# Kernel tuning notes

Hardware: AMD Instinct MI355X
Metric: run time of the kernel (lower is better)

The kernel has to match this reference:

```python
import jax, jax.numpy as jnp
import numpy as np
from jax import lax

IN_CH, OUT_CH, K = 64, 64, 3
FAN_IN = 8           # LogicNets-style fan-in per output channel (over C_in*K taps)
IN_SCALE, IN_BITS = 0.0625, 8
OUT_SCALE, OUT_BITS = 0.125, 8


def make_mask(seed=7):
    # Binary mask [OUT_CH, IN_CH, K] with exactly FAN_IN ones per output channel
    rng = np.random.RandomState(seed)
    m = np.zeros((OUT_CH, IN_CH * K), dtype=np.float32)
    for o in range(OUT_CH):
        idx = rng.choice(IN_CH * K, size=FAN_IN, replace=False)
        m[o, idx] = 1.0
    return jnp.asarray(m.reshape(OUT_CH, IN_CH, K))


def fake_quant(v, scale, bits):
    # symmetric fake quantization with straight-through estimator
    qmin = -(2 ** (bits - 1))
    qmax = 2 ** (bits - 1) - 1
    q = jnp.clip(jnp.round(v / scale), qmin, qmax) * scale
    return v + lax.stop_gradient(q - v)


def setup_inputs() -> dict:
    key = jax.random.key(0)
    k1, k2 = jax.random.split(key)
    x = jax.random.normal(k1, (512, IN_CH, 1024), dtype=jnp.float32)
    weight = jax.random.normal(k2, (OUT_CH, IN_CH, K), dtype=jnp.float32) * 0.1
    mask = make_mask()
    return {"x": x, "weight": weight, "mask": mask}


def reference(x, weight, mask):
    # input quant
    xq = fake_quant(x, IN_SCALE, IN_BITS)
    # masked (sparse) conv1d, padding=1 (same length)
    w = weight * mask
    out = lax.conv_general_dilated(
        xq, w,
        window_strides=(1,),
        padding=[(1, 1)],
        dimension_numbers=("NCH", "OIH", "NCH"),
    )
    # output quant
    return fake_quant(out, OUT_SCALE, OUT_BITS)
```

## Files before the change

kernel.cpp:

```cpp
#include <hip/hip_runtime.h>

namespace {
constexpr int kInCh  = 64;
constexpr int kOutCh = 64;
constexpr int kK     = 3;
constexpr int kFanIn = 8;
constexpr int kH     = 1024;
constexpr int kTile  = 64;
constexpr int kRow   = 72;
constexpr int kWaves = 4;
constexpr int kBlk   = 64 * kWaves;
constexpr int kHB    = kH / kTile;
constexpr int kGridB = 512;
}

struct Tap { int off; float w; };

__device__ __forceinline__ float quant_in_i(float v) {
    float q = rintf(v * 16.0f);
    q = fmaxf(q, -128.0f);
    return fminf(q, 127.0f);
}

__device__ __forceinline__ float quant_out(float v) {
    float q = rintf(v * 8.0f);
    q = fmaxf(q, -128.0f);
    q = fminf(q, 127.0f);
    return q * 0.125f;
}

__global__ void prep_taps(const float* __restrict__ weight,
                          const float* __restrict__ mask,
                          Tap* __restrict__ taps) {
    __shared__ unsigned long long bal[3];
    const int o    = blockIdx.x;
    const int j    = threadIdx.x;
    const int k    = j >> 6;
    const int ci   = j & 63;
    const int idx  = (o * kInCh + ci) * kK + k;

    const float m = mask[idx];
    const unsigned long long b = __ballot(m != 0.0f);
    if (ci == 0) bal[k] = b;
    __syncthreads();

    const unsigned long long lower = b & ((1ull << ci) - 1ull);
    int rank = __popcll(lower);
    #pragma unroll
    for (int w = 0; w < kK; ++w) if (w < k) rank += __popcll(bal[w]);

    if (m != 0.0f && rank < kFanIn) {
        taps[o * kFanIn + rank].off = ci * kRow + k + 3;
        taps[o * kFanIn + rank].w   = weight[idx] * m * 0.0625f;
    }
    int total = __popcll(bal[0]) + __popcll(bal[1]) + __popcll(bal[2]);
    if (j >= total && j < kFanIn) {
        taps[o * kFanIn + j].off = 3;
        taps[o * kFanIn + j].w   = 0.0f;
    }
}

__device__ __forceinline__ void issue_loads(const float* __restrict__ x, int tau,
                                            int lane, float4* __restrict__ r,
                                            float& hl, float& hr) {
    const int n  = tau >> 4;
    const int h0 = (tau & (kHB - 1)) * kTile;
    const float* __restrict__ p = x + ((size_t)n * kInCh) * kH + h0;
    #pragma unroll
    for (int i = 0; i < 16; ++i) {
        const int f = i * 64 + lane;
        r[i] = reinterpret_cast<const float4*>(p + (f >> 4) * kH)[f & 15];
    }
    hl = 0.f; hr = 0.f;
    if (h0 > 0)          hl = p[lane * kH - 1];
    if (h0 + kTile < kH) hr = p[lane * kH + kTile];
}

__device__ __forceinline__ void stage(float (* __restrict__ my)[kRow], int lane,
                                      const float4* __restrict__ r, float hl, float hr) {
    #pragma unroll
    for (int i = 0; i < 16; ++i) {
        const int f = i * 64 + lane;
        float4 q;
        q.x = quant_in_i(r[i].x); q.y = quant_in_i(r[i].y);
        q.z = quant_in_i(r[i].z); q.w = quant_in_i(r[i].w);
        *reinterpret_cast<float4*>(&my[f >> 4][4 + (f & 15) * 4]) = q;
    }
    my[lane][3]         = quant_in_i(hl);
    my[lane][4 + kTile] = quant_in_i(hr);
}

__global__ __launch_bounds__(kBlk, 2) void sparse_conv(
        const float* __restrict__ x,
        const Tap*   __restrict__ taps,
        float*       __restrict__ out,
        int nTiles, int strideW) {
    __shared__ float sm[kWaves][kInCh][kRow];

    const int t    = threadIdx.x;
    const int lane = t & 63;
    const int g    = __builtin_amdgcn_readfirstlane(t >> 6);
    float (* __restrict__ my)[kRow] = sm[g];
    const float* __restrict__ smf = &my[0][0];

    int tau = blockIdx.x * kWaves + g;
    float4 r[16]; float hl, hr;
    if (tau < nTiles) issue_loads(x, tau, lane, r, hl, hr);

    while (tau < nTiles) {
        stage(my, lane, r, hl, hr);
        const int cur = tau;
        tau += strideW;
        if (tau < nTiles) issue_loads(x, tau, lane, r, hl, hr);

        const int n  = cur >> 4;
        const int h0 = (cur & (kHB - 1)) * kTile;
        float* __restrict__ outn = out + ((size_t)n * kOutCh) * kH + h0;

        #pragma unroll 8
        for (int o = 0; o < kOutCh; ++o) {
            const Tap* __restrict__ tp = taps + o * kFanIn;
            float acc = 0.f;
            #pragma unroll
            for (int j = 0; j < kFanIn; ++j)
                acc = fmaf(tp[j].w, smf[tp[j].off + lane], acc);
            outn[(size_t)o * kH + lane] = quant_out(acc);
        }
    }
}

extern "C" void kernel_launch(void* const* d_in, const int* in_sizes, int n_in,
                              void* d_out, int out_size, void* d_ws, size_t ws_size,
                              hipStream_t stream) {
    const float* x      = (const float*)d_in[0];
    const float* weight = (const float*)d_in[1];
    const float* mask   = (const float*)d_in[2];
    float* out = (float*)d_out;
    Tap* taps = (Tap*)d_ws;

    const int nBatch = in_sizes[0] / (kInCh * kH);
    const int nTiles = nBatch * kHB;
    const int strideW = kGridB * kWaves;

    prep_taps<<<kOutCh, kInCh * kK, 0, stream>>>(weight, mask, taps);
    sparse_conv<<<kGridB, kBlk, 0, stream>>>(x, taps, out, nTiles, strideW);
}
```

Measured before the change: 255.6 us.

## Share each input tile across a 512-thread block, splitting output channels over waves

```diff
diff --git a/kernel.cpp b/kernel.cpp
--- a/kernel.cpp
+++ b/kernel.cpp
@@ -8,10 +8,9 @@
 constexpr int kH     = 1024;
 constexpr int kTile  = 64;
 constexpr int kRow   = 72;
-constexpr int kWaves = 4;
-constexpr int kBlk   = 64 * kWaves;
+constexpr int kBlk   = 512;
 constexpr int kHB    = kH / kTile;
-constexpr int kGridB = 512;
+constexpr int kGridB = 2048;
 }
 
 struct Tap { int off; float w; };
@@ -60,73 +59,73 @@
     }
 }
 
-__device__ __forceinline__ void issue_loads(const float* __restrict__ x, int tau,
-                                            int lane, float4* __restrict__ r,
-                                            float& hl, float& hr) {
-    const int n  = tau >> 4;
-    const int h0 = (tau & (kHB - 1)) * kTile;
-    const float* __restrict__ p = x + ((size_t)n * kInCh) * kH + h0;
-    #pragma unroll
-    for (int i = 0; i < 16; ++i) {
-        const int f = i * 64 + lane;
-        r[i] = reinterpret_cast<const float4*>(p + (f >> 4) * kH)[f & 15];
-    }
-    hl = 0.f; hr = 0.f;
-    if (h0 > 0)          hl = p[lane * kH - 1];
-    if (h0 + kTile < kH) hr = p[lane * kH + kTile];
-}
-
-__device__ __forceinline__ void stage(float (* __restrict__ my)[kRow], int lane,
-                                      const float4* __restrict__ r, float hl, float hr) {
-    #pragma unroll
-    for (int i = 0; i < 16; ++i) {
-        const int f = i * 64 + lane;
-        float4 q;
-        q.x = quant_in_i(r[i].x); q.y = quant_in_i(r[i].y);
-        q.z = quant_in_i(r[i].z); q.w = quant_in_i(r[i].w);
-        *reinterpret_cast<float4*>(&my[f >> 4][4 + (f & 15) * 4]) = q;
-    }
-    my[lane][3]         = quant_in_i(hl);
-    my[lane][4 + kTile] = quant_in_i(hr);
-}
-
-__global__ __launch_bounds__(kBlk, 2) void sparse_conv(
+__global__ __launch_bounds__(kBlk, 8) void sparse_conv(
         const float* __restrict__ x,
         const Tap*   __restrict__ taps,
         float*       __restrict__ out,
-        int nTiles, int strideW) {
-    __shared__ float sm[kWaves][kInCh][kRow];
+        int nTiles, int stride) {
+    __shared__ float sm[2][kInCh * kRow];
 
     const int t    = threadIdx.x;
     const int lane = t & 63;
     const int g    = __builtin_amdgcn_readfirstlane(t >> 6);
-    float (* __restrict__ my)[kRow] = sm[g];
-    const float* __restrict__ smf = &my[0][0];
+    const int ci0  = t >> 4;
+    const int c4   = t & 15;
 
-    int tau = blockIdx.x * kWaves + g;
-    float4 r[16]; float hl, hr;
-    if (tau < nTiles) issue_loads(x, tau, lane, r, hl, hr);
+    float4 r0, r1; float hl = 0.f;
+    int tau = blockIdx.x;
+
+#define ISSUE(TAU)                                                                 \
+    {                                                                              \
+        const int n_  = (TAU) >> 4;                                                \
+        const int h0_ = ((TAU) & (kHB - 1)) * kTile;                               \
+        const float* __restrict__ p_ = x + ((size_t)n_ * kInCh) * kH + h0_;        \
+        r0 = reinterpret_cast<const float4*>(p_ + ci0 * kH)[c4];                   \
+        r1 = reinterpret_cast<const float4*>(p_ + (ci0 + 32) * kH)[c4];            \
+        hl = 0.f;                                                                  \
+        if (t < 64)       { if (h0_ > 0)          hl = p_[t * kH - 1]; }           \
+        else if (t < 128) { if (h0_ + kTile < kH) hl = p_[(t - 64) * kH + kTile]; }\
+    }
+
+    ISSUE(tau);
+    int p = 0;
 
     while (tau < nTiles) {
-        stage(my, lane, r, hl, hr);
+        float* __restrict__ buf = sm[p];
+        {
+            float4 q;
+            q.x = quant_in_i(r0.x); q.y = quant_in_i(r0.y);
+            q.z = quant_in_i(r0.z); q.w = quant_in_i(r0.w);
+            reinterpret_cast<float4*>(&buf[ci0 * kRow + 4])[c4] = q;
+            q.x = quant_in_i(r1.x); q.y = quant_in_i(r1.y);
+            q.z = quant_in_i(r1.z); q.w = quant_in_i(r1.w);
+            reinterpret_cast<float4*>(&buf[(ci0 + 32) * kRow + 4])[c4] = q;
+            if (t < 64)       buf[t * kRow + 3] = quant_in_i(hl);
+            else if (t < 128) buf[(t - 64) * kRow + 4 + kTile] = quant_in_i(hl);
+        }
+        __syncthreads();
+
         const int cur = tau;
-        tau += strideW;
-        if (tau < nTiles) issue_loads(x, tau, lane, r, hl, hr);
+        tau += stride;
+        if (tau < nTiles) ISSUE(tau);
 
         const int n  = cur >> 4;
         const int h0 = (cur & (kHB - 1)) * kTile;
         float* __restrict__ outn = out + ((size_t)n * kOutCh) * kH + h0;
 
-        #pragma unroll 8
-        for (int o = 0; o < kOutCh; ++o) {
+        #pragma unroll 4
+        for (int oo = 0; oo < 8; ++oo) {
+            const int o = g * 8 + oo;
             const Tap* __restrict__ tp = taps + o * kFanIn;
             float acc = 0.f;
             #pragma unroll
             for (int j = 0; j < kFanIn; ++j)
-                acc = fmaf(tp[j].w, smf[tp[j].off + lane], acc);
+                acc = fmaf(tp[j].w, buf[tp[j].off + lane], acc);
             outn[(size_t)o * kH + lane] = quant_out(acc);
         }
+        p ^= 1;
     }
+#undef ISSUE
 }
 
 extern "C" void kernel_launch(void* const* d_in, const int* in_sizes, int n_in,
@@ -140,8 +139,8 @@
 
     const int nBatch = in_sizes[0] / (kInCh * kH);
     const int nTiles = nBatch * kHB;
-    const int strideW = kGridB * kWaves;
+    const int grid   = nTiles < kGridB ? nTiles : kGridB;
 
     prep_taps<<<kOutCh, kInCh * kK, 0, stream>>>(weight, mask, taps);
-    sparse_conv<<<kGridB, kBlk, 0, stream>>>(x, taps, out, nTiles, strideW);
+    sparse_conv<<<grid, kBlk, 0, stream>>>(x, taps, out, nTiles, grid);
 }
```

New measurement: 240.9 us. 1.06x faster.
